# Kernel optimization log

Hardware: AMD Instinct MI355X
Metric: run time of the kernel (lower is better)

Reference implementation:

```python
import jax, jax.numpy as jnp
import numpy as np

B, D, N, S = 4096, 768, 8192, 4  # batch, embedding_dim, len(y)==cat rows, source_size


def setup_inputs() -> dict:
    key = jax.random.key(0)
    k1, k2, k3, k4 = jax.random.split(key, 4)
    batch_x = jax.random.normal(k1, (B, D), dtype=jnp.float32)
    cat = jax.random.normal(k2, (N, D), dtype=jnp.float32)
    y = jax.random.randint(k3, (N,), 0, 2, dtype=jnp.int32)
    # phi_srcs: xavier-uniform-like scale for (D, 1) params, stacked as [S, D]
    phi = jax.random.normal(k4, (S, D), dtype=jnp.float32) * 0.05
    bias = jnp.zeros((1,), dtype=jnp.float32)
    return {"batch_x": batch_x, "cat": cat, "y": y, "phi": phi, "bias": bias}


def reference(batch_x, cat, y, phi, bias):
    # con[n, b] = cat[n] . batch_x[b]   -> [N, B]
    con = jnp.einsum('nd,bd->nb', cat, batch_x)
    # F.normalize(con, p=4, dim=0): divide each column by its 4-norm (eps=1e-12)
    norm4 = jnp.power(jnp.sum(jnp.abs(con) ** 4, axis=0), 0.25)
    con = con / jnp.maximum(norm4, 1e-12)
    # softmax over all N rows (dim=0), per batch column
    con = jax.nn.softmax(con, axis=0)
    # chunk into S sources along the N axis: psi [S, N/S, B]
    psi = con.reshape(S, N // S, B)
    yf = y.astype(jnp.float32).reshape(S, N // S)  # y chunks [S, N/S]
    # theta_s = exp(x @ phi_s): [S, B]  (unnormalized, as in the original output path)
    theta = jnp.exp(jnp.einsum('bd,sd->sb', batch_x, phi))
    # per-source: sum_n y[s,n] * psi[s,n,b], then scale by theta[s,b]; sum over sources
    sum_matrix = jnp.sum(jnp.einsum('sn,snb->sb', yf, psi) * theta, axis=0)  # [B]
    y_hat = jax.nn.sigmoid(sum_matrix + bias)  # bias [1] broadcasts -> [B]
    return y_hat
```

## Files before the change

kernel.cpp:

```cpp
#include <hip/hip_runtime.h>
#include <hip/hip_bf16.h>
#include <stdint.h>

#define Bdim 4096
#define Ddim 768
#define Ndim 8192
#define Sdim 4

typedef __attribute__((ext_vector_type(8))) short short8;
typedef __attribute__((ext_vector_type(4))) float floatx4;

__device__ inline unsigned short f2bf(float f) {
  unsigned u = __builtin_bit_cast(unsigned, f);
  unsigned r = (u + 0x7fffu + ((u >> 16) & 1u)) >> 16;
  return (unsigned short)r;
}
__device__ inline float bf2f(unsigned short s) {
  return __builtin_bit_cast(float, (unsigned)s << 16);
}

__device__ inline void async_copy16(const void* g, void* l) {
  __builtin_amdgcn_global_load_lds(
      (__attribute__((address_space(1))) void*)(g),
      (__attribute__((address_space(3))) void*)(l),
      16, 0, 0);
}

__global__ void convert_kernel(const float* __restrict__ x,
                               const float* __restrict__ cat,
                               unsigned short* __restrict__ xb,
                               unsigned short* __restrict__ catb,
                               float* __restrict__ stats) {
  int gid = blockIdx.x * blockDim.x + threadIdx.x;
  int stride = gridDim.x * blockDim.x;
  const int nx4 = (Bdim * Ddim) / 4;
  const int nc4 = (Ndim * Ddim) / 4;
  for (int i = gid; i < nx4; i += stride) {
    float4 v = ((const float4*)x)[i];
    ushort4 o;
    o.x = f2bf(v.x); o.y = f2bf(v.y); o.z = f2bf(v.z); o.w = f2bf(v.w);
    ((ushort4*)xb)[i] = o;
  }
  for (int i = gid; i < nc4; i += stride) {
    float4 v = ((const float4*)cat)[i];
    ushort4 o;
    o.x = f2bf(v.x); o.y = f2bf(v.y); o.z = f2bf(v.z); o.w = f2bf(v.w);
    ((ushort4*)catb)[i] = o;
  }
  if (gid < 6 * Bdim) stats[gid] = 0.0f;
}

__global__ __launch_bounds__(256) void gemm_bt_kernel(
    const unsigned short* __restrict__ A,
    const unsigned short* __restrict__ Bm,
    unsigned short* __restrict__ C) {
  __shared__ unsigned short As[128 * 32];
  __shared__ unsigned short Bs[128 * 32];

  const int tid = threadIdx.x;
  const int wave = tid >> 6;
  const int lane = tid & 63;
  const int quad = lane >> 4;
  const int l16 = lane & 15;
  const int wm = (wave & 1) * 64;
  const int wn = (wave >> 1) * 64;
  const int m0 = blockIdx.x * 128;
  const int n0 = blockIdx.y * 128;

  floatx4 acc[4][4];
#pragma unroll
  for (int i = 0; i < 4; ++i)
#pragma unroll
    for (int j = 0; j < 4; ++j) acc[i][j] = (floatx4){0.f, 0.f, 0.f, 0.f};

  const int c0 = tid, c1 = tid + 256;
  const int r0 = c0 >> 2, col0 = (c0 & 3) * 8;
  const int r1 = c1 >> 2, col1 = (c1 & 3) * 8;
  const unsigned short* a0 = A + (size_t)(m0 + r0) * Ddim + col0;
  const unsigned short* a1 = A + (size_t)(m0 + r1) * Ddim + col1;
  const unsigned short* b0 = Bm + (size_t)(n0 + r0) * Ddim + col0;
  const unsigned short* b1 = Bm + (size_t)(n0 + r1) * Ddim + col1;

  for (int k0 = 0; k0 < Ddim; k0 += 32) {
    async_copy16(a0 + k0, (char*)As + c0 * 16);
    async_copy16(a1 + k0, (char*)As + c1 * 16);
    async_copy16(b0 + k0, (char*)Bs + c0 * 16);
    async_copy16(b1 + k0, (char*)Bs + c1 * 16);
    __syncthreads();

    short8 af[4], bf[4];
#pragma unroll
    for (int mi = 0; mi < 4; ++mi)
      af[mi] = *(const short8*)(As + (wm + mi * 16 + l16) * 32 + quad * 8);
#pragma unroll
    for (int ni = 0; ni < 4; ++ni)
      bf[ni] = *(const short8*)(Bs + (wn + ni * 16 + l16) * 32 + quad * 8);
#pragma unroll
    for (int mi = 0; mi < 4; ++mi)
#pragma unroll
      for (int ni = 0; ni < 4; ++ni)
        acc[mi][ni] = __builtin_amdgcn_mfma_f32_16x16x32_bf16(
            af[mi], bf[ni], acc[mi][ni], 0, 0, 0);
    __syncthreads();
  }

#pragma unroll
  for (int mi = 0; mi < 4; ++mi)
#pragma unroll
    for (int ni = 0; ni < 4; ++ni) {
      int row = m0 + wm + mi * 16 + quad * 4;
      int col = n0 + wn + ni * 16 + l16;
#pragma unroll
      for (int r = 0; r < 4; ++r)
        C[(size_t)(row + r) * Bdim + col] = f2bf(acc[mi][ni][r]);
    }
}

__global__ void pow4_kernel(const unsigned short* __restrict__ con,
                            float* __restrict__ s4) {
  int b = blockIdx.x * 256 + threadIdx.x;
  int n0 = blockIdx.y * 128;
  const unsigned short* p = con + (size_t)n0 * Bdim + b;
  float acc = 0.f;
#pragma unroll 4
  for (int i = 0; i < 128; ++i) {
    float c = bf2f(p[(size_t)i * Bdim]);
    float c2 = c * c;
    acc += c2 * c2;
  }
  atomicAdd(&s4[b], acc);
}

__global__ void expsum_kernel(const unsigned short* __restrict__ con,
                              const float* __restrict__ s4,
                              const int* __restrict__ y,
                              float* __restrict__ denom,
                              float* __restrict__ numer) {
  int b = blockIdx.x * 256 + threadIdx.x;
  int n0 = blockIdx.y * 128;
  int src = n0 / (Ndim / Sdim);
  float nrm = sqrtf(sqrtf(s4[b]));
  float inv = 1.0f / fmaxf(nrm, 1e-12f);
  const unsigned short* p = con + (size_t)n0 * Bdim + b;
  float dsum = 0.f, nsum = 0.f;
#pragma unroll 4
  for (int i = 0; i < 128; ++i) {
    float e = __expf(bf2f(p[(size_t)i * Bdim]) * inv);
    dsum += e;
    nsum += e * (float)y[n0 + i];
  }
  atomicAdd(&denom[b], dsum);
  atomicAdd(&numer[src * Bdim + b], nsum);
}

__global__ void finalize_kernel(const float* __restrict__ x,
                                const float* __restrict__ phi,
                                const float* __restrict__ denom,
                                const float* __restrict__ numer,
                                const float* __restrict__ bias,
                                float* __restrict__ out) {
  int gw = (blockIdx.x * blockDim.x + threadIdx.x) >> 6;
  int lane = threadIdx.x & 63;
  if (gw >= Bdim) return;
  const float* xr = x + (size_t)gw * Ddim;
  float a0 = 0.f, a1 = 0.f, a2 = 0.f, a3 = 0.f;
  for (int d = lane; d < Ddim; d += 64) {
    float xv = xr[d];
    a0 = fmaf(xv, phi[d], a0);
    a1 = fmaf(xv, phi[Ddim + d], a1);
    a2 = fmaf(xv, phi[2 * Ddim + d], a2);
    a3 = fmaf(xv, phi[3 * Ddim + d], a3);
  }
#pragma unroll
  for (int off = 32; off > 0; off >>= 1) {
    a0 += __shfl_down(a0, off);
    a1 += __shfl_down(a1, off);
    a2 += __shfl_down(a2, off);
    a3 += __shfl_down(a3, off);
  }
  if (lane == 0) {
    float s = numer[gw] * __expf(a0) + numer[Bdim + gw] * __expf(a1) +
              numer[2 * Bdim + gw] * __expf(a2) + numer[3 * Bdim + gw] * __expf(a3);
    s = s / denom[gw];
    float z = s + bias[0];
    out[gw] = 1.0f / (1.0f + __expf(-z));
  }
}

extern "C" void kernel_launch(void* const* d_in, const int* in_sizes, int n_in,
                              void* d_out, int out_size, void* d_ws,
                              size_t ws_size, hipStream_t stream) {
  const float* batch_x = (const float*)d_in[0];
  const float* cat = (const float*)d_in[1];
  const int* y = (const int*)d_in[2];
  const float* phi = (const float*)d_in[3];
  const float* bias = (const float*)d_in[4];
  float* out = (float*)d_out;

  char* ws = (char*)d_ws;
  unsigned short* catb = (unsigned short*)ws;
  unsigned short* xb = catb + (size_t)Ndim * Ddim;
  unsigned short* con = xb + (size_t)Bdim * Ddim;
  float* stats = (float*)(con + (size_t)Ndim * Bdim);
  float* s4 = stats;
  float* denom = s4 + Bdim;
  float* numer = denom + Bdim;

  convert_kernel<<<2048, 256, 0, stream>>>(batch_x, cat, xb, catb, stats);

  dim3 g2(Ndim / 128, Bdim / 128);
  gemm_bt_kernel<<<g2, 256, 0, stream>>>(catb, xb, con);

  dim3 g3(Bdim / 256, Ndim / 128);
  pow4_kernel<<<g3, 256, 0, stream>>>(con, s4);
  expsum_kernel<<<g3, 256, 0, stream>>>(con, s4, y, denom, numer);

  finalize_kernel<<<1024, 256, 0, stream>>>(batch_x, phi, denom, numer, bias, out);
}
```

Before: 191.8 us.

## Fuse pow4 reduction into GEMM epilogue, swizzle LDS, vectorize expsum

The column 4-norm accumulation moves into the GEMM epilogue, using fp32 accumulators, wave shuffles and atomics, so the separate pow4 pass that re-read the whole con matrix is gone. The global-to-LDS copy and fragment reads now use an XOR swizzle on the k-chunk to reduce LDS bank conflicts. The expsum kernel now handles four columns per thread with ushort4 loads and 64-row chunks. The norm is now computed from unrounded fp32 values instead of bf16, which changes numerics slightly, and the epilogue adds more atomics.

```diff
diff --git a/kernel.cpp b/kernel.cpp
--- a/kernel.cpp
+++ b/kernel.cpp
@@ -53,7 +53,8 @@
 __global__ __launch_bounds__(256) void gemm_bt_kernel(
     const unsigned short* __restrict__ A,
     const unsigned short* __restrict__ Bm,
-    unsigned short* __restrict__ C) {
+    unsigned short* __restrict__ C,
+    float* __restrict__ s4) {
   __shared__ unsigned short As[128 * 32];
   __shared__ unsigned short Bs[128 * 32];
 
@@ -74,12 +75,16 @@
     for (int j = 0; j < 4; ++j) acc[i][j] = (floatx4){0.f, 0.f, 0.f, 0.f};
 
   const int c0 = tid, c1 = tid + 256;
-  const int r0 = c0 >> 2, col0 = (c0 & 3) * 8;
-  const int r1 = c1 >> 2, col1 = (c1 & 3) * 8;
-  const unsigned short* a0 = A + (size_t)(m0 + r0) * Ddim + col0;
-  const unsigned short* a1 = A + (size_t)(m0 + r1) * Ddim + col1;
-  const unsigned short* b0 = Bm + (size_t)(n0 + r0) * Ddim + col0;
-  const unsigned short* b1 = Bm + (size_t)(n0 + r1) * Ddim + col1;
+  const int r0 = c0 >> 2, r1 = c1 >> 2;
+  const int j0 = (c0 & 3) ^ (r0 & 3) ^ ((r0 >> 2) & 3);
+  const int j1 = (c1 & 3) ^ (r1 & 3) ^ ((r1 >> 2) & 3);
+  const unsigned short* a0 = A + (size_t)(m0 + r0) * Ddim + j0 * 8;
+  const unsigned short* a1 = A + (size_t)(m0 + r1) * Ddim + j1 * 8;
+  const unsigned short* b0 = Bm + (size_t)(n0 + r0) * Ddim + j0 * 8;
+  const unsigned short* b1 = Bm + (size_t)(n0 + r1) * Ddim + j1 * 8;
+
+  const int fl = (l16 & 3) ^ ((l16 >> 2) & 3);
+  const int ksw = (quad ^ fl) * 8;
 
   for (int k0 = 0; k0 < Ddim; k0 += 32) {
     async_copy16(a0 + k0, (char*)As + c0 * 16);
@@ -91,10 +96,10 @@
     short8 af[4], bf[4];
 #pragma unroll
     for (int mi = 0; mi < 4; ++mi)
-      af[mi] = *(const short8*)(As + (wm + mi * 16 + l16) * 32 + quad * 8);
+      af[mi] = *(const short8*)(As + (wm + mi * 16 + l16) * 32 + ksw);
 #pragma unroll
     for (int ni = 0; ni < 4; ++ni)
-      bf[ni] = *(const short8*)(Bs + (wn + ni * 16 + l16) * 32 + quad * 8);
+      bf[ni] = *(const short8*)(Bs + (wn + ni * 16 + l16) * 32 + ksw);
 #pragma unroll
     for (int mi = 0; mi < 4; ++mi)
 #pragma unroll
@@ -104,6 +109,7 @@
     __syncthreads();
   }
 
+  float cs4[4] = {0.f, 0.f, 0.f, 0.f};
 #pragma unroll
   for (int mi = 0; mi < 4; ++mi)
 #pragma unroll
@@ -111,24 +117,20 @@
       int row = m0 + wm + mi * 16 + quad * 4;
       int col = n0 + wn + ni * 16 + l16;
 #pragma unroll
-      for (int r = 0; r < 4; ++r)
-        C[(size_t)(row + r) * Bdim + col] = f2bf(acc[mi][ni][r]);
+      for (int r = 0; r < 4; ++r) {
+        float c = acc[mi][ni][r];
+        C[(size_t)(row + r) * Bdim + col] = f2bf(c);
+        float c2 = c * c;
+        cs4[ni] += c2 * c2;
+      }
     }
-}
-
-__global__ void pow4_kernel(const unsigned short* __restrict__ con,
-                            float* __restrict__ s4) {
-  int b = blockIdx.x * 256 + threadIdx.x;
-  int n0 = blockIdx.y * 128;
-  const unsigned short* p = con + (size_t)n0 * Bdim + b;
-  float acc = 0.f;
-#pragma unroll 4
-  for (int i = 0; i < 128; ++i) {
-    float c = bf2f(p[(size_t)i * Bdim]);
-    float c2 = c * c;
-    acc += c2 * c2;
-  }
-  atomicAdd(&s4[b], acc);
+#pragma unroll
+  for (int ni = 0; ni < 4; ++ni) {
+    float v = cs4[ni];
+    v += __shfl_xor(v, 16);
+    v += __shfl_xor(v, 32);
+    if (quad == 0) atomicAdd(&s4[n0 + wn + ni * 16 + l16], v);
+  }
 }
 
 __global__ void expsum_kernel(const unsigned short* __restrict__ con,
@@ -136,21 +138,39 @@
                               const int* __restrict__ y,
                               float* __restrict__ denom,
                               float* __restrict__ numer) {
-  int b = blockIdx.x * 256 + threadIdx.x;
-  int n0 = blockIdx.y * 128;
+  int col0 = blockIdx.x * 1024 + threadIdx.x * 4;
+  int n0 = blockIdx.y * 64;
   int src = n0 / (Ndim / Sdim);
-  float nrm = sqrtf(sqrtf(s4[b]));
-  float inv = 1.0f / fmaxf(nrm, 1e-12f);
-  const unsigned short* p = con + (size_t)n0 * Bdim + b;
-  float dsum = 0.f, nsum = 0.f;
-#pragma unroll 4
-  for (int i = 0; i < 128; ++i) {
-    float e = __expf(bf2f(p[(size_t)i * Bdim]) * inv);
-    dsum += e;
-    nsum += e * (float)y[n0 + i];
-  }
-  atomicAdd(&denom[b], dsum);
-  atomicAdd(&numer[src * Bdim + b], nsum);
+
+  float4 s = *(const float4*)(s4 + col0);
+  float inv0 = 1.0f / fmaxf(sqrtf(sqrtf(s.x)), 1e-12f);
+  float inv1 = 1.0f / fmaxf(sqrtf(sqrtf(s.y)), 1e-12f);
+  float inv2 = 1.0f / fmaxf(sqrtf(sqrtf(s.z)), 1e-12f);
+  float inv3 = 1.0f / fmaxf(sqrtf(sqrtf(s.w)), 1e-12f);
+
+  const unsigned short* p = con + (size_t)n0 * Bdim + col0;
+  float d0 = 0.f, d1 = 0.f, d2 = 0.f, d3 = 0.f;
+  float m0 = 0.f, m1 = 0.f, m2 = 0.f, m3 = 0.f;
+#pragma unroll 8
+  for (int i = 0; i < 64; ++i) {
+    ushort4 v = *(const ushort4*)(p + (size_t)i * Bdim);
+    float yv = (float)y[n0 + i];
+    float e0 = __expf(bf2f(v.x) * inv0);
+    float e1 = __expf(bf2f(v.y) * inv1);
+    float e2 = __expf(bf2f(v.z) * inv2);
+    float e3 = __expf(bf2f(v.w) * inv3);
+    d0 += e0; d1 += e1; d2 += e2; d3 += e3;
+    m0 += e0 * yv; m1 += e1 * yv; m2 += e2 * yv; m3 += e3 * yv;
+  }
+  atomicAdd(&denom[col0 + 0], d0);
+  atomicAdd(&denom[col0 + 1], d1);
+  atomicAdd(&denom[col0 + 2], d2);
+  atomicAdd(&denom[col0 + 3], d3);
+  float* np = numer + (size_t)src * Bdim + col0;
+  atomicAdd(np + 0, m0);
+  atomicAdd(np + 1, m1);
+  atomicAdd(np + 2, m2);
+  atomicAdd(np + 3, m3);
 }
 
 __global__ void finalize_kernel(const float* __restrict__ x,
@@ -209,10 +229,9 @@
   convert_kernel<<<2048, 256, 0, stream>>>(batch_x, cat, xb, catb, stats);
 
   dim3 g2(Ndim / 128, Bdim / 128);
-  gemm_bt_kernel<<<g2, 256, 0, stream>>>(catb, xb, con);
-
-  dim3 g3(Bdim / 256, Ndim / 128);
-  pow4_kernel<<<g3, 256, 0, stream>>>(con, s4);
+  gemm_bt_kernel<<<g2, 256, 0, stream>>>(catb, xb, con, s4);
+
+  dim3 g3(Bdim / 1024, Ndim / 64);
   expsum_kernel<<<g3, 256, 0, stream>>>(con, s4, y, denom, numer);
 
   finalize_kernel<<<1024, 256, 0, stream>>>(batch_x, phi, denom, numer, bias, out);
```

After: 193.0 us. No clear change (+0.6%).
